# Kernel tuning notes

Measured on AMD Instinct MI355X. Metric: run time of the kernel, lower is better.

The kernel has to match this reference:

```python
import jax, jax.numpy as jnp
import numpy as np


def setup_inputs() -> dict:
    key = jax.random.key(0)
    k1, k2 = jax.random.split(key)
    B, H, S = 16, 512, 1024          # batch, hidden=nd*embed_dim, seqlen
    ND, ED, K = 4, 128, 4096         # nd, embed_dim, num_embed
    inputs = jax.random.normal(k1, (B, H, S), dtype=jnp.float32)
    embeddings = jax.random.normal(k2, (ND, ED, K), dtype=jnp.float32)
    return {"inputs": inputs, "embeddings": embeddings}


def reference(inputs, embeddings):
    # VectorQuant.forward with soft_train=False, gsoftmax=False, EMA=False (VQ-VAE straight-through path)
    commit_cost = 0.25
    B, H, S = inputs.shape
    ND, ED, K = embeddings.shape
    # stack_enc_outputs: (B, H, S) -> (B*S, nd, embed_dim) via contiguous view (C-order reshape)
    enc = inputs.reshape(B * S, ND, ED)
    x2 = jnp.sum(enc * enc, axis=2, keepdims=True)            # (BS, nd, 1)
    e2 = jnp.sum(embeddings * embeddings, axis=1)[None]       # (1, nd, K)
    cross = jnp.einsum('dhk,bdh->bdk', embeddings, enc)       # (BS, nd, K)
    distances = x2 + e2 - 2.0 * cross
    # per-token, per-chunk nearest code
    latents = jnp.argmin(distances, axis=2).T                 # (nd, BS)
    # gather codebook vectors: embeddings[d][:, latents[d]] -> (nd, ED, BS)
    encodings = jnp.take_along_axis(embeddings, latents[:, None, :], axis=2)
    # split_outputs: (nd, ED, B*S) -> (B, H, S) via contiguous view (C-order reshape)
    encodings = encodings.reshape(B, H, S)
    # straight-through estimator
    output = inputs + jax.lax.stop_gradient(encodings) - jax.lax.stop_gradient(inputs)
    commit_loss = jnp.mean((inputs - jax.lax.stop_gradient(encodings)) ** 2)
    loss = commit_cost * commit_loss
    kl = jnp.asarray(0, dtype=jnp.int32)
    return (output, loss, commit_loss, kl)
```

## Files before the change

### kernel.cpp

```cpp
#include <hip/hip_runtime.h>

#define ND 4
#define ED 128
#define KCODES 4096
#define NTOK 16384
#define HID 512
#define NTOT (ND*ED*NTOK)

#define MARGIN 2.0e-3f
#define FLAG_CAP 16384

typedef __attribute__((ext_vector_type(8))) short short8v;
typedef __attribute__((ext_vector_type(4))) float float4v;

#define GLDS16(g, l) __builtin_amdgcn_global_load_lds( \
    (const __attribute__((address_space(1))) unsigned int*)(g), \
    (__attribute__((address_space(3))) unsigned int*)(l), 16, 0, 0)

__device__ __forceinline__ unsigned short bf16h(float x) {
    unsigned u = __float_as_uint(x);
    return (unsigned short)((u + 0x7fffu + ((u >> 16) & 1u)) >> 16);
}
__device__ __forceinline__ float bf16f(unsigned short h) {
    return __uint_as_float(((unsigned)h) << 16);
}

__global__ __launch_bounds__(256) void e2split_kernel(const float* __restrict__ emb,
        float* __restrict__ e2g, unsigned short* __restrict__ bfrag,
        int* __restrict__ flag_cnt) {
    __shared__ float Tf[128][17];
    const int tile = blockIdx.x;
    const int d    = blockIdx.y;
    const int tid  = threadIdx.x;
    const int k0   = tile * 16;
    if (tile == 0 && d == 0 && tid == 0) *flag_cnt = 0;
    {
        int e = tid >> 1, half = tid & 1;
        const float* src = emb + ((size_t)d * ED + e) * KCODES + k0 + half * 8;
        float4 v0 = *(const float4*)(src);
        float4 v1 = *(const float4*)(src + 4);
        float* dst = &Tf[e][half * 8];
        dst[0] = v0.x; dst[1] = v0.y; dst[2] = v0.z; dst[3] = v0.w;
        dst[4] = v1.x; dst[5] = v1.y; dst[6] = v1.z; dst[7] = v1.w;
    }
    __syncthreads();
    if (tid < 16) {
        float s = 0.f;
        for (int e = 0; e < ED; ++e) {
            float v = Tf[e][tid];
            s = __fadd_rn(s, __fmul_rn(v, v));
        }
        e2g[d * KCODES + k0 + tid] = s;
    }
    #pragma unroll
    for (int q = 0; q < 2; ++q) {
        int c    = q * 256 + tid;
        int arr  = c >> 8;
        int rem  = c & 255;
        int code = rem >> 4;
        int kpos = rem & 15;
        int e0   = (kpos ^ code) * 8;
        short8v v;
        #pragma unroll
        for (int j = 0; j < 8; ++j) {
            float x = Tf[e0 + j][code];
            unsigned short hb = bf16h(x);
            v[j] = arr ? (short)bf16h(x - bf16f(hb)) : (short)hb;
        }
        size_t idx = ((size_t)(d * 256 + tile)) * 4096 + arr * 2048 + code * 128 + kpos * 8;
        *(short8v*)(bfrag + idx) = v;
    }
}

__global__ __launch_bounds__(256, 2)
void argmin_mfma_kernel(const float* __restrict__ in,
        const unsigned short* __restrict__ bfrag, const float* __restrict__ e2g,
        int* __restrict__ lat, int* __restrict__ flag_cnt, int* __restrict__ flag_list) {
    __shared__ __align__(16) char LB[49152];

    const int l   = blockIdx.x;
    const int r8  = l & 7;
    const int d   = r8 >> 1;
    const int tI  = 2 * (l >> 3) + (r8 & 1);
    const int t0  = tI * 128;

    const int tid  = threadIdx.x;
    const int w    = tid >> 6;
    const int lane = tid & 63;
    const int l15  = lane & 15;
    const int lk8  = lane >> 4;

    float* e2p = (float*)(LB + 32768);
    #pragma unroll
    for (int i = 0; i < 16; ++i) {
        int idx = i * 256 + tid;
        e2p[idx] = e2g[d * KCODES + idx] + 512.0f;
    }

    short8v ahf[2][4], alf[2][4];
    #pragma unroll
    for (int rt = 0; rt < 2; ++rt) {
        const float* ap = in + (size_t)(t0 + w * 32 + rt * 16 + l15) * HID + d * ED + lk8 * 8;
        #pragma unroll
        for (int ks = 0; ks < 4; ++ks) {
            float4 v0 = *(const float4*)(ap + ks * 32);
            float4 v1 = *(const float4*)(ap + ks * 32 + 4);
            float vv[8] = {v0.x, v0.y, v0.z, v0.w, v1.x, v1.y, v1.z, v1.w};
            short8v hv, lv;
            #pragma unroll
            for (int j = 0; j < 8; ++j) {
                unsigned short hb = bf16h(vv[j]);
                hv[j] = (short)hb;
                lv[j] = (short)bf16h(vv[j] - bf16f(hb));
            }
            ahf[rt][ks] = hv; alf[rt][ks] = lv;
        }
    }

    int fo[4];
    #pragma unroll
    for (int ks = 0; ks < 4; ++ks)
        fo[ks] = l15 * 256 + (((ks * 4 + lk8) ^ l15) * 16);

    const char* sb = (const char*)bfrag + ((size_t)(d * 256)) * 8192 + tid * 16;

    #pragma unroll
    for (int t = 0; t < 2; ++t) {
        GLDS16(sb + t * 8192,        LB + t * 8192 + w * 1024);
        GLDS16(sb + t * 8192 + 4096, LB + t * 8192 + 4096 + w * 1024);
    }
    __syncthreads();

    unsigned m1[2][4], m2[2][4];
    int bk[2][4];
    #pragma unroll
    for (int rt = 0; rt < 2; ++rt)
        #pragma unroll
        for (int r = 0; r < 4; ++r) { m1[rt][r] = 0xFFFFFFFFu; m2[rt][r] = 0xFFFFFFFFu; bk[rt][r] = 0; }

    #pragma unroll 4
    for (int s = 0; s < 256; ++s) {
        if (s < 254) {
            const char* sp = sb + (size_t)(s + 2) * 8192;
            char* dp = LB + ((s + 2) & 3) * 8192 + w * 1024;
            GLDS16(sp,        dp);
            GLDS16(sp + 4096, dp + 4096);
        }
        const char* cur = LB + (s & 3) * 8192;
        const float e2v = e2p[s * 16 + l15];

        float4v aP[2] = {{0,0,0,0},{0,0,0,0}};
        float4v aQ[2] = {{0,0,0,0},{0,0,0,0}};
        #pragma unroll
        for (int ks = 0; ks < 4; ++ks) {
            short8v bh = *(const short8v*)(cur + fo[ks]);
            short8v bl = *(const short8v*)(cur + 4096 + fo[ks]);
            aP[0] = __builtin_amdgcn_mfma_f32_16x16x32_bf16(ahf[0][ks], bh, aP[0], 0, 0, 0);
            aP[1] = __builtin_amdgcn_mfma_f32_16x16x32_bf16(ahf[1][ks], bh, aP[1], 0, 0, 0);
            aP[0] = __builtin_amdgcn_mfma_f32_16x16x32_bf16(alf[0][ks], bh, aP[0], 0, 0, 0);
            aP[1] = __builtin_amdgcn_mfma_f32_16x16x32_bf16(alf[1][ks], bh, aP[1], 0, 0, 0);
            aQ[0] = __builtin_amdgcn_mfma_f32_16x16x32_bf16(ahf[0][ks], bl, aQ[0], 0, 0, 0);
            aQ[1] = __builtin_amdgcn_mfma_f32_16x16x32_bf16(ahf[1][ks], bl, aQ[1], 0, 0, 0);
        }
        #pragma unroll
        for (int rt = 0; rt < 2; ++rt) {
            #pragma unroll
            for (int r = 0; r < 4; ++r) {
                float cs = aP[rt][r] + aQ[rt][r];
                float dv = __fmaf_rn(-2.0f, cs, e2v);
                unsigned kk = __float_as_uint(dv);
                unsigned mo = m1[rt][r];
                unsigned mx = mo > kk ? mo : kk;
                m2[rt][r] = m2[rt][r] < mx ? m2[rt][r] : mx;
                if (kk < mo) { bk[rt][r] = s; m1[rt][r] = kk; }
            }
        }
        if (s < 254)        asm volatile("s_waitcnt vmcnt(2)" ::: "memory");
        else if (s == 254)  asm volatile("s_waitcnt vmcnt(0)" ::: "memory");
        __builtin_amdgcn_s_barrier();
    }

    #pragma unroll
    for (int rt = 0; rt < 2; ++rt) {
        #pragma unroll
        for (int r = 0; r < 4; ++r) {
            unsigned long long key = ((unsigned long long)m1[rt][r] << 32) |
                                     (unsigned)(bk[rt][r] * 16 + l15);
            unsigned mm2 = m2[rt][r];
            #pragma unroll
            for (int m = 1; m <= 8; m <<= 1) {
                unsigned long long ok = __shfl_xor(key, m, 64);
                unsigned om = __shfl_xor(mm2, m, 64);
                unsigned loser = (ok < key) ? (unsigned)(key >> 32) : (unsigned)(ok >> 32);
                key = ok < key ? ok : key;
                unsigned t2 = om < loser ? om : loser;
                mm2 = mm2 < t2 ? mm2 : t2;
            }
            if (l15 == 0) {
                int code = (int)(key & 0xFFFFu);
                int tok = d * NTOK + t0 + w * 32 + rt * 16 + lk8 * 4 + r;
                lat[tok] = code;
                float gap = __uint_as_float(mm2) - __uint_as_float((unsigned)(key >> 32));
                if (gap < MARGIN) {
                    int slot = atomicAdd(flag_cnt, 1);
                    if (slot < FLAG_CAP) flag_list[slot] = tok;
                }
            }
        }
    }
}

__global__ __launch_bounds__(256) void repair_kernel(const float* __restrict__ in,
        const float* __restrict__ emb, const float* __restrict__ e2g,
        const int* __restrict__ flag_cnt, const int* __restrict__ flag_list,
        int* __restrict__ lat) {
    __shared__ float xs[ED];
    __shared__ float rd[256];
    __shared__ int   rk[256];
    int n = *flag_cnt;
    if (n > FLAG_CAP) n = FLAG_CAP;
    for (int idx = blockIdx.x; idx < n; idx += gridDim.x) {
        int tok = flag_list[idx];
        int d = tok >> 14;
        int t = tok & (NTOK - 1);
        __syncthreads();
        if (threadIdx.x < ED) xs[threadIdx.x] = in[(size_t)t * HID + d * ED + threadIdx.x];
        __syncthreads();
        float x2v = 0.f;
        for (int e = 0; e < ED; ++e) x2v = __fadd_rn(x2v, __fmul_rn(xs[e], xs[e]));
        const float* __restrict__ embd = emb + (size_t)d * ED * KCODES;
        float bd = 3.0e38f; int bkk = 0;
        for (int j = 0; j < 16; ++j) {
            int k = threadIdx.x + j * 256;
            float acc = 0.f;
            #pragma unroll 16
            for (int e = 0; e < ED; ++e)
                acc = __fmaf_rn(xs[e], embd[(size_t)e * KCODES + k], acc);
            float dist = __fsub_rn(__fadd_rn(x2v, e2g[d * KCODES + k]),
                                   __fmul_rn(2.0f, acc));
            if (dist < bd) { bd = dist; bkk = k; }
        }
        rd[threadIdx.x] = bd; rk[threadIdx.x] = bkk;
        __syncthreads();
        for (int w = 128; w > 0; w >>= 1) {
            if (threadIdx.x < w) {
                float od = rd[threadIdx.x + w]; int ok = rk[threadIdx.x + w];
                if (od < rd[threadIdx.x] || (od == rd[threadIdx.x] && ok < rk[threadIdx.x])) {
                    rd[threadIdx.x] = od; rk[threadIdx.x] = ok;
                }
            }
            __syncthreads();
        }
        if (threadIdx.x == 0) lat[tok] = rk[0];
    }
}

__global__ __launch_bounds__(256) void gather_kernel(const float* __restrict__ in,
        const float* __restrict__ emb, const int* __restrict__ lat,
        float* __restrict__ out, float* __restrict__ partial) {
    int tid  = threadIdx.x;
    int base = blockIdx.x * 1024 + tid * 4;
    int d = base >> 21;
    int e = (base >> 14) & 127;
    int t = base & (NTOK - 1);
    const int4 kk = *(const int4*)(lat + d * NTOK + t);
    const float* __restrict__ row = emb + ((size_t)(d * ED + e)) * KCODES;
    float enc[4];
    enc[0] = row[kk.x]; enc[1] = row[kk.y]; enc[2] = row[kk.z]; enc[3] = row[kk.w];
    const float4 x = *(const float4*)(in + base);
    const float xv[4] = {x.x, x.y, x.z, x.w};
    float4 ov; float* o = (float*)&ov;
    float s = 0.f;
    #pragma unroll
    for (int i = 0; i < 4; ++i) {
        o[i] = __fsub_rn(__fadd_rn(xv[i], enc[i]), xv[i]);
        float df = xv[i] - enc[i];
        s = __fmaf_rn(df, df, s);
    }
    *(float4*)(out + base) = ov;
    #pragma unroll
    for (int off = 32; off > 0; off >>= 1) s += __shfl_down(s, off, 64);
    __shared__ float wsum[4];
    if ((tid & 63) == 0) wsum[tid >> 6] = s;
    __syncthreads();
    if (tid == 0) partial[blockIdx.x] = wsum[0] + wsum[1] + wsum[2] + wsum[3];
}

__global__ __launch_bounds__(256) void finalize_kernel(const float* __restrict__ partial,
                                                       float* __restrict__ out_tail) {
    __shared__ double sh[256];
    double s = 0.0;
    for (int i = threadIdx.x; i < 8192; i += 256) s += (double)partial[i];
    sh[threadIdx.x] = s;
    __syncthreads();
    for (int w = 128; w > 0; w >>= 1) {
        if (threadIdx.x < w) sh[threadIdx.x] += sh[threadIdx.x + w];
        __syncthreads();
    }
    if (threadIdx.x == 0) {
        double mean = sh[0] / (double)NTOT;
        out_tail[0] = (float)(0.25 * mean);
        out_tail[1] = (float)mean;
        ((int*)out_tail)[2] = 0;
    }
}

extern "C" void kernel_launch(void* const* d_in, const int* in_sizes, int n_in,
                              void* d_out, int out_size, void* d_ws, size_t ws_size,
                              hipStream_t stream) {
    const float* in  = (const float*)d_in[0];
    const float* emb = (const float*)d_in[1];
    float* out = (float*)d_out;
    char* ws = (char*)d_ws;

    int*   lat       = (int*)ws;
    float* e2g       = (float*)(ws + 262144);
    float* partial   = (float*)(ws + 327680);
    int*   flag_cnt  = (int*)(ws + 360448);
    int*   flag_list = (int*)(ws + 360452);
    unsigned short* bfrag = (unsigned short*)(ws + (1 << 20));

    hipLaunchKernelGGL(e2split_kernel, dim3(256, 4), dim3(256), 0, stream,
                       emb, e2g, bfrag, flag_cnt);
    hipLaunchKernelGGL(argmin_mfma_kernel, dim3(512), dim3(256), 0, stream,
                       in, bfrag, e2g, lat, flag_cnt, flag_list);
    hipLaunchKernelGGL(repair_kernel, dim3(64), dim3(256), 0, stream,
                       in, emb, e2g, flag_cnt, flag_list, lat);
    hipLaunchKernelGGL(gather_kernel, dim3(NTOT / 1024), dim3(256), 0, stream,
                       in, emb, lat, out, partial);
    hipLaunchKernelGGL(finalize_kernel, dim3(1), dim3(256), 0, stream, partial, out + NTOT);
}
```

Baseline: 273.6 us.

## Split argmin codebook scan in halves across blocks and merge partial results

```diff
diff --git a/kernel.cpp b/kernel.cpp
--- a/kernel.cpp
+++ b/kernel.cpp
@@ -75,13 +75,14 @@
 __global__ __launch_bounds__(256, 2)
 void argmin_mfma_kernel(const float* __restrict__ in,
         const unsigned short* __restrict__ bfrag, const float* __restrict__ e2g,
-        int* __restrict__ lat, int* __restrict__ flag_cnt, int* __restrict__ flag_list) {
-    __shared__ __align__(16) char LB[49152];
+        unsigned long long* __restrict__ pk, unsigned* __restrict__ pm2) {
+    __shared__ __align__(16) char LB[40960];
 
     const int l   = blockIdx.x;
     const int r8  = l & 7;
     const int d   = r8 >> 1;
-    const int tI  = 2 * (l >> 3) + (r8 & 1);
+    const int h   = r8 & 1;
+    const int tI  = l >> 3;
     const int t0  = tI * 128;
 
     const int tid  = threadIdx.x;
@@ -92,9 +93,9 @@
 
     float* e2p = (float*)(LB + 32768);
     #pragma unroll
-    for (int i = 0; i < 16; ++i) {
+    for (int i = 0; i < 8; ++i) {
         int idx = i * 256 + tid;
-        e2p[idx] = e2g[d * KCODES + idx] + 512.0f;
+        e2p[idx] = e2g[d * KCODES + h * 2048 + idx] + 512.0f;
     }
 
     short8v ahf[2][4], alf[2][4];
@@ -122,7 +123,7 @@
     for (int ks = 0; ks < 4; ++ks)
         fo[ks] = l15 * 256 + (((ks * 4 + lk8) ^ l15) * 16);
 
-    const char* sb = (const char*)bfrag + ((size_t)(d * 256)) * 8192 + tid * 16;
+    const char* sb = (const char*)bfrag + ((size_t)(d * 256 + h * 128)) * 8192 + tid * 16;
 
     #pragma unroll
     for (int t = 0; t < 2; ++t) {
@@ -139,8 +140,8 @@
         for (int r = 0; r < 4; ++r) { m1[rt][r] = 0xFFFFFFFFu; m2[rt][r] = 0xFFFFFFFFu; bk[rt][r] = 0; }
 
     #pragma unroll 4
-    for (int s = 0; s < 256; ++s) {
-        if (s < 254) {
+    for (int s = 0; s < 128; ++s) {
+        if (s < 126) {
             const char* sp = sb + (size_t)(s + 2) * 8192;
             char* dp = LB + ((s + 2) & 3) * 8192 + w * 1024;
             GLDS16(sp,        dp);
@@ -151,6 +152,7 @@
 
         float4v aP[2] = {{0,0,0,0},{0,0,0,0}};
         float4v aQ[2] = {{0,0,0,0},{0,0,0,0}};
+        __builtin_amdgcn_s_setprio(1);
         #pragma unroll
         for (int ks = 0; ks < 4; ++ks) {
             short8v bh = *(const short8v*)(cur + fo[ks]);
@@ -162,6 +164,7 @@
             aQ[0] = __builtin_amdgcn_mfma_f32_16x16x32_bf16(ahf[0][ks], bl, aQ[0], 0, 0, 0);
             aQ[1] = __builtin_amdgcn_mfma_f32_16x16x32_bf16(ahf[1][ks], bl, aQ[1], 0, 0, 0);
         }
+        __builtin_amdgcn_s_setprio(0);
         #pragma unroll
         for (int rt = 0; rt < 2; ++rt) {
             #pragma unroll
@@ -175,8 +178,8 @@
                 if (kk < mo) { bk[rt][r] = s; m1[rt][r] = kk; }
             }
         }
-        if (s < 254)        asm volatile("s_waitcnt vmcnt(2)" ::: "memory");
-        else if (s == 254)  asm volatile("s_waitcnt vmcnt(0)" ::: "memory");
+        if (s < 126)        asm volatile("s_waitcnt vmcnt(2)" ::: "memory");
+        else if (s == 126)  asm volatile("s_waitcnt vmcnt(0)" ::: "memory");
         __builtin_amdgcn_s_barrier();
     }
 
@@ -185,7 +188,7 @@
         #pragma unroll
         for (int r = 0; r < 4; ++r) {
             unsigned long long key = ((unsigned long long)m1[rt][r] << 32) |
-                                     (unsigned)(bk[rt][r] * 16 + l15);
+                                     (unsigned)(h * 2048 + bk[rt][r] * 16 + l15);
             unsigned mm2 = m2[rt][r];
             #pragma unroll
             for (int m = 1; m <= 8; m <<= 1) {
@@ -197,16 +200,30 @@
                 mm2 = mm2 < t2 ? mm2 : t2;
             }
             if (l15 == 0) {
-                int code = (int)(key & 0xFFFFu);
                 int tok = d * NTOK + t0 + w * 32 + rt * 16 + lk8 * 4 + r;
-                lat[tok] = code;
-                float gap = __uint_as_float(mm2) - __uint_as_float((unsigned)(key >> 32));
-                if (gap < MARGIN) {
-                    int slot = atomicAdd(flag_cnt, 1);
-                    if (slot < FLAG_CAP) flag_list[slot] = tok;
-                }
-            }
-        }
+                pk[(size_t)h * 65536 + tok] = key;
+                pm2[(size_t)h * 65536 + tok] = mm2;
+            }
+        }
+    }
+}
+
+__global__ __launch_bounds__(256) void merge_kernel(
+        const unsigned long long* __restrict__ pk, const unsigned* __restrict__ pm2,
+        int* __restrict__ lat, int* __restrict__ flag_cnt, int* __restrict__ flag_list) {
+    int tok = blockIdx.x * 256 + threadIdx.x;
+    unsigned long long ka = pk[tok], kb = pk[65536 + tok];
+    unsigned m2a = pm2[tok], m2b = pm2[65536 + tok];
+    bool aw = ka < kb;
+    unsigned long long kw = aw ? ka : kb;
+    unsigned loser1 = (unsigned)((aw ? kb : ka) >> 32);
+    unsigned m2w = aw ? m2a : m2b;
+    unsigned B2 = m2w < loser1 ? m2w : loser1;
+    lat[tok] = (int)(kw & 0xFFFFu);
+    float gap = __uint_as_float(B2) - __uint_as_float((unsigned)(kw >> 32));
+    if (gap < MARGIN) {
+        int slot = atomicAdd(flag_cnt, 1);
+        if (slot < FLAG_CAP) flag_list[slot] = tok;
     }
 }
 
@@ -318,12 +335,16 @@
     float* partial   = (float*)(ws + 327680);
     int*   flag_cnt  = (int*)(ws + 360448);
     int*   flag_list = (int*)(ws + 360452);
-    unsigned short* bfrag = (unsigned short*)(ws + (1 << 20));
+    unsigned long long* pk  = (unsigned long long*)(ws + 458752);
+    unsigned*           pm2 = (unsigned*)(ws + 1572864);
+    unsigned short* bfrag = (unsigned short*)(ws + 2097152);
 
     hipLaunchKernelGGL(e2split_kernel, dim3(256, 4), dim3(256), 0, stream,
                        emb, e2g, bfrag, flag_cnt);
-    hipLaunchKernelGGL(argmin_mfma_kernel, dim3(512), dim3(256), 0, stream,
-                       in, bfrag, e2g, lat, flag_cnt, flag_list);
+    hipLaunchKernelGGL(argmin_mfma_kernel, dim3(1024), dim3(256), 0, stream,
+                       in, bfrag, e2g, pk, pm2);
+    hipLaunchKernelGGL(merge_kernel, dim3(256), dim3(256), 0, stream,
+                       pk, pm2, lat, flag_cnt, flag_list);
     hipLaunchKernelGGL(repair_kernel, dim3(64), dim3(256), 0, stream,
                        in, emb, e2g, flag_cnt, flag_list, lat);
     hipLaunchKernelGGL(gather_kernel, dim3(NTOT / 1024), dim3(256), 0, stream,
```

Measured after the change: 279.5 us. +2.2%, slower.
